# Kernel optimization log

Measured on AMD Instinct MI355X. Metric: run time of the kernel, lower is better.

The kernel has to match this reference:

```python
import jax, jax.numpy as jnp
import numpy as np

N = 50000        # nodes
E = 800000       # edges
R = 8            # relations
G = 64           # g_dim
H1 = 64          # h1_dim
H2 = 32          # h2_dim (per-head for transformer, output for sage)
HEADS = 4
EPS = 1e-5       # BatchNorm eps


def setup_inputs() -> dict:
    key = jax.random.key(0)
    ks = jax.random.split(key, 16)
    def rn(k, shape, scale=0.05):
        return jax.random.normal(k, shape, dtype=jnp.float32) * scale
    return {
        "node_features": jax.random.normal(ks[0], (N, G), dtype=jnp.float32),
        "node_type": jax.random.randint(ks[1], (N,), 0, 3),
        "edge_index": jax.random.randint(ks[2], (2, E), 0, N),
        "edge_type": jax.random.randint(ks[3], (E,), 0, R),
        # RGCNConv params (per-relation weight + root weight + bias)
        "rgcn_w": rn(ks[4], (R, G, H1)),
        "rgcn_root": rn(ks[5], (G, H1)),
        "rgcn_bias": jnp.zeros((H1,), jnp.float32),
        "bn1_g": jnp.ones((H1,), jnp.float32),
        "bn1_b": jnp.zeros((H1,), jnp.float32),
        # TransformerConv params (q/k/v projections + skip)
        "wq": rn(ks[6], (H1, HEADS * H2)), "bq": jnp.zeros((HEADS * H2,), jnp.float32),
        "wk": rn(ks[7], (H1, HEADS * H2)), "bk": jnp.zeros((HEADS * H2,), jnp.float32),
        "wv": rn(ks[8], (H1, HEADS * H2)), "bv": jnp.zeros((HEADS * H2,), jnp.float32),
        "wskip": rn(ks[9], (H1, HEADS * H2)), "bskip": jnp.zeros((HEADS * H2,), jnp.float32),
        "bn2_g": jnp.ones((HEADS * H2,), jnp.float32),
        "bn2_b": jnp.zeros((HEADS * H2,), jnp.float32),
        # SAGEConv params (lin_l on aggregated neighbors has bias; lin_r on root has none)
        "sage_wl": rn(ks[10], (HEADS * H2, H2)), "sage_bl": jnp.zeros((H2,), jnp.float32),
        "sage_wr": rn(ks[11], (HEADS * H2, H2)),
        "bn3_g": jnp.ones((H2,), jnp.float32),
        "bn3_b": jnp.zeros((H2,), jnp.float32),
    }


def _bn(x, g, b):
    # BatchNorm1d in training mode: biased batch statistics over nodes
    m = x.mean(0)
    v = x.var(0)
    return g * (x - m) * jax.lax.rsqrt(v + EPS) + b


def _match(res, d):
    # F.pad(res, (0, d - c)): pads with zeros if d > c, truncates if d < c
    c = res.shape[1]
    if d > c:
        return jnp.pad(res, ((0, 0), (0, d - c)))
    return res[:, :d]


def _forward(node_features, rgcn_w, rgcn_root, rgcn_bias, bn1_g, bn1_b,
             wq, bq, wk, bk, wv, bv, wskip, bskip, bn2_g, bn2_b,
             sage_wl, sage_bl, sage_wr, bn3_g, bn3_b,
             edge_index, edge_type):
    src, dst = edge_index[0], edge_index[1]
    x = node_features
    residual = x

    # ---- RGCNConv: per-relation transform, per-relation mean aggregation, sum over relations ----
    xr = jnp.einsum('nf,rfh->nrh', x, rgcn_w)            # [N,R,H1]
    msg = xr[src, edge_type]                              # [E,H1]
    seg = dst * R + edge_type                             # segment per (node, relation)
    sums = jax.ops.segment_sum(msg, seg, num_segments=N * R)
    cnt = jax.ops.segment_sum(jnp.ones((E,), msg.dtype), seg, num_segments=N * R)
    agg = (sums / jnp.maximum(cnt, 1.0)[:, None]).reshape(N, R, H1).sum(1)
    h = agg + x @ rgcn_root + rgcn_bias
    h = jax.nn.leaky_relu(_bn(h, bn1_g, bn1_b))
    x = h + _match(residual, h.shape[1])
    residual = x

    # ---- TransformerConv: edge softmax attention, concat heads, + skip projection ----
    q = (x @ wq + bq).reshape(N, HEADS, H2)
    k = (x @ wk + bk).reshape(N, HEADS, H2)
    v = (x @ wv + bv).reshape(N, HEADS, H2)
    logits = (q[dst] * k[src]).sum(-1) / jnp.sqrt(jnp.float32(H2))  # [E,HEADS]
    mx = jax.ops.segment_max(logits, dst, num_segments=N)
    ex = jnp.exp(logits - mx[dst])
    den = jax.ops.segment_sum(ex, dst, num_segments=N)
    alpha = ex / jnp.maximum(den[dst], 1e-16)
    out = jax.ops.segment_sum(alpha[:, :, None] * v[src], dst, num_segments=N)
    h = out.reshape(N, HEADS * H2) + x @ wskip + bskip
    h = jax.nn.leaky_relu(_bn(h, bn2_g, bn2_b))
    x = h + _match(residual, h.shape[1])
    residual = x

    # ---- SAGEConv: mean neighbor aggregation + root transform ----
    nsum = jax.ops.segment_sum(x[src], dst, num_segments=N)
    ncnt = jax.ops.segment_sum(jnp.ones((E,), x.dtype), dst, num_segments=N)
    nmean = nsum / jnp.maximum(ncnt, 1.0)[:, None]
    h = nmean @ sage_wl + sage_bl + x @ sage_wr
    h = jax.nn.leaky_relu(_bn(h, bn3_g, bn3_b))
    return h + _match(residual, h.shape[1])


def reference(node_features, node_type, edge_index, edge_type,
              rgcn_w, rgcn_root, rgcn_bias, bn1_g, bn1_b,
              wq, bq, wk, bk, wv, bv, wskip, bskip, bn2_g, bn2_b,
              sage_wl, sage_bl, sage_wr, bn3_g, bn3_b):
    # node_type is unused by the original forward
    return _forward(node_features, rgcn_w, rgcn_root, rgcn_bias, bn1_g, bn1_b,
                    wq, bq, wk, bk, wv, bv, wskip, bskip, bn2_g, bn2_b,
                    sage_wl, sage_bl, sage_wr, bn3_g, bn3_b,
                    edge_index, edge_type)
```

## Files before the change

kernel.cpp:

```cpp
#include <hip/hip_runtime.h>
#include <stdint.h>

#define NN 50000
#define NE 800000
#define NR (NN*8)
#define SCAN_BS 512
#define NB2 782
#define INV_N (1.0f/50000.0f)
#define BN_EPS 1e-5f

typedef unsigned short ushort_t;
typedef unsigned char uchar_t;
typedef short bf16x8 __attribute__((ext_vector_type(8)));
typedef float f32x4 __attribute__((ext_vector_type(4)));
typedef float f32x2 __attribute__((ext_vector_type(2)));

__device__ __forceinline__ ushort_t f2bf(float f){
    unsigned int u = __float_as_uint(f);
    u += 0x7FFFu + ((u >> 16) & 1u);
    return (ushort_t)(u >> 16);
}
__device__ __forceinline__ float bf2f(ushort_t h){ return __uint_as_float(((unsigned int)h) << 16); }
__device__ __forceinline__ float bflo(unsigned int u){ return __uint_as_float(u << 16); }
__device__ __forceinline__ float bfhi(unsigned int u){ return __uint_as_float(u & 0xFFFF0000u); }

__device__ __forceinline__ unsigned int f4_to_fp8(float a, float b, float c, float d){
    int v = __builtin_amdgcn_cvt_pk_fp8_f32(a, b, 0, false);
    v = __builtin_amdgcn_cvt_pk_fp8_f32(c, d, v, true);
    return (unsigned int)v;
}
__device__ __forceinline__ void fp8_to_f4(unsigned int u, float& a, float& b, float& c, float& d){
    f32x2 lo = __builtin_amdgcn_cvt_pk_f32_fp8(u, false);
    f32x2 hi = __builtin_amdgcn_cvt_pk_f32_fp8(u, true);
    a = lo.x; b = lo.y; c = hi.x; d = hi.y;
}

__global__ void k_deg(const int* __restrict__ ei, const int* __restrict__ et,
                      int* __restrict__ deg, uint2* __restrict__ sr){
    int e = blockIdx.x*256 + threadIdx.x;
    if (e < NE){
        int seg = ei[NE + e]*8 + et[e];
        int rank = atomicAdd(&deg[seg], 1);
        uint2 o; o.x = (unsigned)seg; o.y = (unsigned)rank;
        sr[e] = o;
    }
}

__global__ void k_scan1(const int* __restrict__ deg, int* __restrict__ tmp, int* __restrict__ bsum){
    __shared__ int s[SCAN_BS];
    int t = threadIdx.x;
    int i = blockIdx.x*SCAN_BS + t;
    s[t] = (i < NR) ? deg[i] : 0;
    __syncthreads();
    for (int off = 1; off < SCAN_BS; off <<= 1){
        int add = (t >= off) ? s[t-off] : 0;
        __syncthreads();
        s[t] += add;
        __syncthreads();
    }
    if (i < NR) tmp[i] = s[t];
    if (t == SCAN_BS-1) bsum[blockIdx.x] = s[t];
}

__global__ void k_scan2(int* __restrict__ bsum){
    __shared__ int s[NB2];
    int t = threadIdx.x;
    if (t < NB2) s[t] = bsum[t];
    __syncthreads();
    if (t == 0){
        int acc = 0;
        for (int i = 0; i < NB2; ++i){ acc += s[i]; s[i] = acc; }
    }
    __syncthreads();
    if (t < NB2) bsum[t] = s[t];
}

__global__ void k_scan3(const int* __restrict__ tmp, const int* __restrict__ bsum, int* __restrict__ rs){
    int i = blockIdx.x*256 + threadIdx.x;
    if (i < NR){
        int b = i >> 9;
        int off = (b > 0) ? bsum[b-1] : 0;
        rs[i+1] = tmp[i] + off;
        if (i == 0) rs[0] = 0;
    }
}

__global__ void k_fill(const int* __restrict__ ei, const uint2* __restrict__ sr,
                       const int* __restrict__ rs, int* __restrict__ csr){
    int e = blockIdx.x*256 + threadIdx.x;
    if (e < NE){
        uint2 s = sr[e];
        csr[rs[s.x] + (int)s.y] = ei[e];
    }
}

__global__ void k_prep(const float* __restrict__ nf,
                       const float* __restrict__ rgcn_w, const float* __restrict__ root,
                       const float* __restrict__ wq, const float* __restrict__ wk,
                       const float* __restrict__ wv, const float* __restrict__ wsk,
                       const float* __restrict__ bq, const float* __restrict__ bk,
                       const float* __restrict__ bv, const float* __restrict__ bsk,
                       const float* __restrict__ wl, const float* __restrict__ wr,
                       ushort_t* __restrict__ xb, uchar_t* __restrict__ xb8,
                       ushort_t* __restrict__ Wcat,
                       ushort_t* __restrict__ Wt2, float* __restrict__ bcat,
                       ushort_t* __restrict__ Wsage){
    int i = blockIdx.x*256 + threadIdx.x;
    const int NXB = NN*16;
    if (i < NXB){
        float4 v = ((const float4*)nf)[i];
        ushort4 h;
        h.x = f2bf(v.x); h.y = f2bf(v.y); h.z = f2bf(v.z); h.w = f2bf(v.w);
        ((ushort4*)xb)[i] = h;
        ((unsigned int*)xb8)[i] = f4_to_fp8(v.x, v.y, v.z, v.w);
        return;
    }
    int j = i - NXB;
    if (j < 64*576){
        int h = j / 576, k = j - h*576;
        float v = (k < 512) ? rgcn_w[(size_t)k*64 + h] : root[(size_t)(k-512)*64 + h];
        Wcat[j] = f2bf(v);
    } else if (j < 64*576 + 512*64){
        int jj = j - 64*576;
        int c = jj >> 6, k = jj & 63;
        int mt = c >> 7, cc = c & 127;
        const float* W = (mt==0)?wq:(mt==1)?wk:(mt==2)?wv:wsk;
        Wt2[jj] = f2bf(W[(size_t)k*128 + cc]);
    } else if (j < 64*576 + 512*64 + 512){
        int c = j - (64*576 + 512*64);
        int mt = c >> 7, cc = c & 127;
        const float* B = (mt==0)?bq:(mt==1)?bk:(mt==2)?bv:bsk;
        bcat[c] = B[cc];
    } else if (j < 64*576 + 512*64 + 512 + 32*256){
        int jj = j - (64*576 + 512*64 + 512);
        int c = jj >> 8, k = jj & 255;
        float v = (k < 128) ? wr[(size_t)k*32 + c] : wl[(size_t)(k-128)*32 + c];
        Wsage[jj] = f2bf(v);
    }
}

__global__ __launch_bounds__(256) void rgcn_fused(const ushort_t* __restrict__ xb,
                                                  const uchar_t* __restrict__ xb8,
                                                  const int* __restrict__ rs,
                                                  const int* __restrict__ csr,
                                                  const ushort_t* __restrict__ Wcat,
                                                  const float* __restrict__ bias,
                                                  float* __restrict__ h1pre){
    __shared__ ushort_t Ml[16*520];
    int w = threadIdx.x >> 6, lane = threadIdx.x & 63;
    int quad = lane >> 4, l4 = lane & 15;
    int row0 = blockIdx.x * 16;
    int n0 = row0 + w*4;
    int rsel = (lane < 9 ? lane : 8);
    int rb = rs[n0*8 + rsel];
    int eb0 = __shfl(rb, 0);
    int dg0 = __shfl(rb, 8) - eb0;
    int idx = (lane < dg0) ? csr[eb0 + lane] : 0;
    for (int j = 0; j < 4; ++j){
        int lrow = (w*4 + j)*520;
        int ebase = __shfl(rb, 0);
        int enext = __shfl(rb, 8);
        int rb_next = 0, idxn = 0;
        if (j < 3){
            rb_next = rs[(n0 + j + 1)*8 + rsel];
            idxn = csr[min(enext + lane, NE - 1)];
        }
        int e0a = __shfl(rb, quad),     e1a = __shfl(rb, quad + 1);
        int e0b = __shfl(rb, quad + 4), e1b = __shfl(rb, quad + 5);
        int oa = e0a - ebase, la = e1a - e0a;
        int ob = e0b - ebase, lb = e1b - e0b;
        int ml = max(la, lb);
        ml = max(ml, __shfl_xor(ml, 16));
        ml = max(ml, __shfl_xor(ml, 32));
        float aa0=0.f, aa1=0.f, aa2=0.f, aa3=0.f;
        float ab0=0.f, ab1=0.f, ab2=0.f, ab3=0.f;
        for (int i = 0; i < ml; i += 4){
            int sA[4], sB[4];
            bool vA[4], vB[4];
#pragma unroll
            for (int u = 0; u < 4; ++u){
                int jA = oa + i + u, jB = ob + i + u;
                vA[u] = (i + u) < la;
                vB[u] = (i + u) < lb;
                int tA = __shfl(idx, jA & 63);
                int tB = __shfl(idx, jB & 63);
                if (jA >= 64 && vA[u]) tA = csr[ebase + jA];
                if (jB >= 64 && vB[u]) tB = csr[ebase + jB];
                sA[u] = vA[u] ? tA : 0;
                sB[u] = vB[u] ? tB : 0;
            }
            unsigned int uA[4], uB[4];
#pragma unroll
            for (int u = 0; u < 4; ++u){
                uA[u] = *(const unsigned int*)(xb8 + (size_t)sA[u]*64 + l4*4);
                uB[u] = *(const unsigned int*)(xb8 + (size_t)sB[u]*64 + l4*4);
            }
#pragma unroll
            for (int u = 0; u < 4; ++u){
                float f0,f1,f2,f3;
                fp8_to_f4(uA[u],f0,f1,f2,f3);
                if (vA[u]){ aa0+=f0; aa1+=f1; aa2+=f2; aa3+=f3; }
                fp8_to_f4(uB[u],f0,f1,f2,f3);
                if (vB[u]){ ab0+=f0; ab1+=f1; ab2+=f2; ab3+=f3; }
            }
        }
        float inva = 1.f / fmaxf((float)la, 1.f);
        float invb = 1.f / fmaxf((float)lb, 1.f);
        ushort4 oA, oB;
        oA.x = f2bf(aa0*inva); oA.y = f2bf(aa1*inva); oA.z = f2bf(aa2*inva); oA.w = f2bf(aa3*inva);
        oB.x = f2bf(ab0*invb); oB.y = f2bf(ab1*invb); oB.z = f2bf(ab2*invb); oB.w = f2bf(ab3*invb);
        *(ushort4*)&Ml[lrow + quad*64 + l4*4] = oA;
        *(ushort4*)&Ml[lrow + (quad + 4)*64 + l4*4] = oB;
        if (j < 3){
            rb = rb_next;
            int ebn = __shfl(rb, 0);
            int dgn = __shfl(rb, 8) - ebn;
            idx = (lane < dgn) ? idxn : 0;
        }
    }
    __syncthreads();
    int m = l4;
    f32x4 acc = {};
#pragma unroll
    for (int kt = 0; kt < 18; ++kt){
        int kk = kt*32 + quad*8;
        bf16x8 a;
        if (kt < 16) a = *(const bf16x8*)&Ml[m*520 + kk];
        else         a = *(const bf16x8*)(xb + (size_t)(row0 + m)*64 + (kk - 512));
        bf16x8 b = *(const bf16x8*)(Wcat + (size_t)(w*16 + m)*576 + kk);
        acc = __builtin_amdgcn_mfma_f32_16x16x32_bf16(a, b, acc, 0, 0, 0);
    }
    int col = w*16 + m;
    float bz = bias[col];
#pragma unroll
    for (int i = 0; i < 4; ++i){
        int rr = row0 + quad*4 + i;
        h1pre[(size_t)rr*64 + col] = acc[i] + bz;
    }
}

__global__ void bn1_finalize(const float* __restrict__ sums, const float* __restrict__ sumsq,
                             const float* __restrict__ g1, const float* __restrict__ b1,
                             float* __restrict__ A1, float* __restrict__ C1){
    int c = threadIdx.x;
    if (c < 64){
        float m = sums[c] * INV_N;
        float v = sumsq[c] * INV_N - m*m;
        float rsv = rsqrtf(fmaxf(v, 0.f) + BN_EPS);
        float A = rsv * g1[c];
        A1[c] = A;
        C1[c] = b1[c] - m * A;
    }
}

#define QS 132
#define BS 68
__global__ __launch_bounds__(256) void gemm_qkvs(const float* __restrict__ h1pre,
                                                 const float* __restrict__ nf,
                                                 const float* __restrict__ A1, const float* __restrict__ C1,
                                                 const ushort_t* __restrict__ Wt2,
                                                 const float* __restrict__ bcat,
                                                 ushort_t* __restrict__ qb,
                                                 uchar_t* __restrict__ kb8,
                                                 ushort_t* __restrict__ vb,
                                                 ushort_t* __restrict__ sb){
    __shared__ ushort_t Bs[256*BS];
    __shared__ ushort_t pl[4][16*QS];
    int w = threadIdx.x >> 6, lane = threadIdx.x & 63;
    int m = lane & 15, quad = lane >> 4;
    int r0 = blockIdx.x*64 + w*16;
    int cg = blockIdx.y;
    int row = r0 + m;
    {
        int t = threadIdx.x;
        const ushort_t* wsrc = Wt2 + (size_t)cg*256*64;
#pragma unroll
        for (int u0 = 0; u0 < 8; ++u0){
            int u = u0*256 + t;
            int r = u >> 3, c8 = (u & 7)*8;
            *(uint4*)&Bs[r*BS + c8] = *(const uint4*)(wsrc + u*8);
        }
    }
    bf16x8 afrag[2];
#pragma unroll
    for (int kt = 0; kt < 2; ++kt){
        int db = kt*32 + quad*8;
        bf16x8 f = (bf16x8){0,0,0,0,0,0,0,0};
        if (row < NN){
            float4 h0 = *(const float4*)(h1pre + (size_t)row*64 + db);
            float4 h1 = *(const float4*)(h1pre + (size_t)row*64 + db + 4);
            float4 n0 = *(const float4*)(nf + (size_t)row*64 + db);
            float4 n1 = *(const float4*)(nf + (size_t)row*64 + db + 4);
            float4 a0 = *(const float4*)(A1 + db);
            float4 a1 = *(const float4*)(A1 + db + 4);
            float4 c0 = *(const float4*)(C1 + db);
            float4 c1 = *(const float4*)(C1 + db + 4);
            float hh[8] = {h0.x,h0.y,h0.z,h0.w,h1.x,h1.y,h1.z,h1.w};
            float nn[8] = {n0.x,n0.y,n0.z,n0.w,n1.x,n1.y,n1.z,n1.w};
            float AA[8] = {a0.x,a0.y,a0.z,a0.w,a1.x,a1.y,a1.z,a1.w};
            float CC[8] = {c0.x,c0.y,c0.z,c0.w,c1.x,c1.y,c1.z,c1.w};
#pragma unroll
            for (int e = 0; e < 8; ++e){
                float y = fmaf(hh[e], AA[e], CC[e]);
                y = (y >= 0.f) ? y : 0.01f*y;
                f[e] = (short)f2bf(y + nn[e]);
            }
        }
        afrag[kt] = f;
    }
    __syncthreads();
    f32x4 acc[16] = {};
#pragma unroll
    for (int kt = 0; kt < 2; ++kt){
        int kk = kt*32 + quad*8;
#pragma unroll
        for (int ct = 0; ct < 16; ++ct){
            bf16x8 b = *(const bf16x8*)&Bs[(size_t)(ct*16 + m)*BS + kk];
            acc[ct] = __builtin_amdgcn_mfma_f32_16x16x32_bf16(afrag[kt], b, acc[ct], 0, 0, 0);
        }
    }
#pragma unroll
    for (int ct = 0; ct < 8; ++ct){
        int g = cg*256 + ct*16 + m;
        float bz = bcat[g];
        int cc = g & 127;
#pragma unroll
        for (int i = 0; i < 4; ++i)
            pl[w][(quad*4 + i)*QS + cc] = f2bf(acc[ct][i] + bz);
    }
    if (cg == 0){
#pragma unroll
        for (int t = 0; t < 4; ++t){
            int u = t*64 + lane;
            int r = u >> 4, c = (u & 15)*8;
            int gr = r0 + r;
            if (gr < NN) *(uint4*)(qb + (size_t)gr*128 + c) = *(const uint4*)&pl[w][r*QS + c];
        }
    } else {
#pragma unroll
        for (int t = 0; t < 4; ++t){
            int u = t*64 + lane;
            int r = u >> 4, c = (u & 15)*8;
            int gr = r0 + r;
            if (gr < NN) *(uint4*)(vb + (size_t)gr*128 + c) = *(const uint4*)&pl[w][r*QS + c];
        }
    }
#pragma unroll
    for (int ct = 8; ct < 16; ++ct){
        int g = cg*256 + ct*16 + m;
        float bz = bcat[g];
        int cc = g & 127;
#pragma unroll
        for (int i = 0; i < 4; ++i)
            pl[w][(quad*4 + i)*QS + cc] = f2bf(acc[ct][i] + bz);
    }
    if (cg == 0){
#pragma unroll
        for (int t = 0; t < 4; ++t){
            int u = t*64 + lane;
            int r = u >> 4, c = (u & 15)*8;
            int gr = r0 + r;
            if (gr < NN){
                uint4 kk4 = *(const uint4*)&pl[w][r*QS + c];
                uint2 o;
                o.x = f4_to_fp8(bflo(kk4.x), bfhi(kk4.x), bflo(kk4.y), bfhi(kk4.y));
                o.y = f4_to_fp8(bflo(kk4.z), bfhi(kk4.z), bflo(kk4.w), bfhi(kk4.w));
                *(uint2*)(kb8 + (size_t)gr*128 + c) = o;
            }
        }
    } else {
#pragma unroll
        for (int t = 0; t < 4; ++t){
            int u = t*64 + lane;
            int r = u >> 4, c = (u & 15)*8;
            int gr = r0 + r;
            if (gr < NN) *(uint4*)(sb + (size_t)gr*128 + c) = *(const uint4*)&pl[w][r*QS + c];
        }
    }
}

__global__ __launch_bounds__(256) void sage_gemm(const ushort_t* __restrict__ x2b,
                                                 const ushort_t* __restrict__ nmeanb,
                                                 const ushort_t* __restrict__ Wsage,
                                                 const float* __restrict__ bl,
                                                 float* __restrict__ h3){
    int wv = threadIdx.x >> 6, lane = threadIdx.x & 63;
    int r0 = blockIdx.x*64 + wv*16;
    int m = lane & 15, quad = lane >> 4;
    int row = r0 + m;
    f32x4 acc[2] = {};
#pragma unroll
    for (int kt = 0; kt < 8; ++kt){
        int kk = kt*32 + quad*8;
        bf16x8 a;
        if (row < NN){
            const ushort_t* ap = (kt < 4) ? (x2b + (size_t)row*128 + kk)
                                          : (nmeanb + (size_t)row*128 + (kk - 128));
            a = *(const bf16x8*)ap;
        } else {
            a = (bf16x8){0,0,0,0,0,0,0,0};
        }
#pragma unroll
        for (int ct = 0; ct < 2; ++ct){
            bf16x8 b = *(const bf16x8*)(Wsage + (size_t)(ct*16 + m)*256 + kk);
            acc[ct] = __builtin_amdgcn_mfma_f32_16x16x32_bf16(a, b, acc[ct], 0, 0, 0);
        }
    }
#pragma unroll
    for (int ct = 0; ct < 2; ++ct){
        int col = ct*16 + m;
        float bz = bl[col];
#pragma unroll
        for (int i = 0; i < 4; ++i){
            int rr = r0 + quad*4 + i;
            if (rr < NN) h3[(size_t)rr*32 + col] = acc[ct][i] + bz;
        }
    }
}

template<int C>
__global__ __launch_bounds__(256) void bn_stats(const float* __restrict__ X, int ld,
                                                float* __restrict__ sums, float* __restrict__ sumsq){
    __shared__ float s1[256], s2[256];
    int t = threadIdx.x;
    int c = t & (C-1);
    const int rpb = 256 / C;
    int r = blockIdx.x * rpb + (t / C);
    int rstride = gridDim.x * rpb;
    float a = 0.f, b = 0.f;
    for (; r < NN; r += rstride){
        float v = X[(size_t)r*ld + c];
        a += v; b += v*v;
    }
    s1[t] = a; s2[t] = b;
    __syncthreads();
    for (int off = 128; off >= C; off >>= 1){
        if (t < off){ s1[t] += s1[t+off]; s2[t] += s2[t+off]; }
        __syncthreads();
    }
    if (t < C){ atomicAdd(&sums[t], s1[t]); atomicAdd(&sumsq[t], s2[t]); }
}

__device__ __forceinline__ float bn_leaky(float z, float m, float rsv, float g, float b){
    float y = (z - m) * rsv * g + b;
    return y >= 0.f ? y : 0.01f * y;
}

__global__ void bn_apply2(const float* __restrict__ h2, const float* __restrict__ h1pre,
                          const float* __restrict__ nf,
                          const float* __restrict__ g1, const float* __restrict__ b1,
                          const float* __restrict__ s1, const float* __restrict__ q1,
                          const float* __restrict__ g2, const float* __restrict__ b2,
                          const float* __restrict__ s2, const float* __restrict__ q2,
                          float* __restrict__ x2r, ushort_t* __restrict__ x2b,
                          uchar_t* __restrict__ x28){
    int i = blockIdx.x*256 + threadIdx.x;
    if (i >= NN*128) return;
    int n = i >> 7, c = i & 127;
    float m2 = s2[c] * INV_N;
    float v2 = q2[c] * INV_N - m2*m2;
    float rsv2 = rsqrtf(fmaxf(v2, 0.f) + BN_EPS);
    float val = bn_leaky(h2[i], m2, rsv2, g2[c], b2[c]);
    if (c < 64){
        float m1 = s1[c] * INV_N;
        float v1 = q1[c] * INV_N - m1*m1;
        float rsv1 = rsqrtf(fmaxf(v1, 0.f) + BN_EPS);
        val += bn_leaky(h1pre[(size_t)n*64 + c], m1, rsv1, g1[c], b1[c]) + nf[(size_t)n*64 + c];
    }
    if (c < 32) x2r[(size_t)n*32 + c] = val;
    x2b[i] = f2bf(val);
    int p = __builtin_amdgcn_cvt_pk_fp8_f32(val, val, 0, false);
    x28[i] = (uchar_t)(p & 0xFF);
}

__global__ void bn_apply3(const float* __restrict__ h3, const float* __restrict__ x2r,
                          const float* __restrict__ g, const float* __restrict__ b,
                          const float* __restrict__ sums, const float* __restrict__ sumsq,
                          float* __restrict__ out){
    int i = blockIdx.x*256 + threadIdx.x;
    if (i >= NN*32) return;
    int c = i & 31;
    float m = sums[c] * INV_N;
    float v = sumsq[c] * INV_N - m*m;
    float rsv = rsqrtf(fmaxf(v, 0.f) + BN_EPS);
    out[i] = bn_leaky(h3[i], m, rsv, g[c], b[c]) + x2r[i];
}

__global__ __launch_bounds__(256) void attn_kernel(const ushort_t* __restrict__ qb,
                                                   const uchar_t* __restrict__ kb8,
                                                   const ushort_t* __restrict__ vb,
                                                   const ushort_t* __restrict__ sb,
                                                   const int* __restrict__ rs,
                                                   const int* __restrict__ csr,
                                                   float* __restrict__ h2){
    int w = threadIdx.x >> 6, lane = threadIdx.x & 63;
    int n = blockIdx.x*4 + w;
    if (n >= NN) return;
    int half = lane >> 5, l5 = lane & 31;
    int e0 = rs[n*8], e1 = rs[n*8 + 8];
    int deg = e1 - e0;
    uint2 qu = *(const uint2*)(qb + (size_t)n*128 + l5*4);
    uint2 sbv = *(const uint2*)(sb + (size_t)n*128 + l5*4);
    float q0 = bflo(qu.x), q1 = bfhi(qu.x), q2 = bflo(qu.y), q3 = bfhi(qu.y);
    const float scale = 0.17677669529663687f;
    int idx = 0;
    if (lane < deg) idx = csr[e0 + lane];
    int dcap = min(deg, 64);
    int nt = (dcap + 7) >> 3;
    float den = 0.f, a0 = 0.f, a1 = 0.f, a2 = 0.f, a3 = 0.f;
    for (int t = 0; t < nt; ++t){
        int i2 = t*8 + half*4;
        int j0 = i2, j1 = i2+1, j2 = i2+2, j3 = i2+3;
        bool v0 = j0 < dcap, v1 = j1 < dcap, v2 = j2 < dcap, v3 = j3 < dcap;
        int s0 = __shfl(idx, j0 & 63); s0 = v0 ? s0 : 0;
        int s1 = __shfl(idx, j1 & 63); s1 = v1 ? s1 : 0;
        int s2 = __shfl(idx, j2 & 63); s2 = v2 ? s2 : 0;
        int s3 = __shfl(idx, j3 & 63); s3 = v3 ? s3 : 0;
        unsigned int ku0 = *(const unsigned int*)(kb8 + (size_t)s0*128 + l5*4);
        unsigned int ku1 = *(const unsigned int*)(kb8 + (size_t)s1*128 + l5*4);
        unsigned int ku2 = *(const unsigned int*)(kb8 + (size_t)s2*128 + l5*4);
        unsigned int ku3 = *(const unsigned int*)(kb8 + (size_t)s3*128 + l5*4);
        uint2 vv0 = *(const uint2*)(vb + (size_t)s0*128 + l5*4);
        uint2 vv1 = *(const uint2*)(vb + (size_t)s1*128 + l5*4);
        uint2 vv2 = *(const uint2*)(vb + (size_t)s2*128 + l5*4);
        uint2 vv3 = *(const uint2*)(vb + (size_t)s3*128 + l5*4);
        float ka, kb_, kc, kd;
        fp8_to_f4(ku0, ka, kb_, kc, kd);
        float p0 = q0*ka + q1*kb_ + q2*kc + q3*kd;
        fp8_to_f4(ku1, ka, kb_, kc, kd);
        float p1 = q0*ka + q1*kb_ + q2*kc + q3*kd;
        fp8_to_f4(ku2, ka, kb_, kc, kd);
        float p2 = q0*ka + q1*kb_ + q2*kc + q3*kd;
        fp8_to_f4(ku3, ka, kb_, kc, kd);
        float p3 = q0*ka + q1*kb_ + q2*kc + q3*kd;
        p0 += __shfl_xor(p0, 1); p1 += __shfl_xor(p1, 1); p2 += __shfl_xor(p2, 1); p3 += __shfl_xor(p3, 1);
        p0 += __shfl_xor(p0, 2); p1 += __shfl_xor(p1, 2); p2 += __shfl_xor(p2, 2); p3 += __shfl_xor(p3, 2);
        p0 += __shfl_xor(p0, 4); p1 += __shfl_xor(p1, 4); p2 += __shfl_xor(p2, 4); p3 += __shfl_xor(p3, 4);
        float w0 = v0 ? __expf(p0 * scale) : 0.f;
        float w1 = v1 ? __expf(p1 * scale) : 0.f;
        float w2 = v2 ? __expf(p2 * scale) : 0.f;
        float w3 = v3 ? __expf(p3 * scale) : 0.f;
        den += w0 + w1 + w2 + w3;
        a0 += w0*bflo(vv0.x) + w1*bflo(vv1.x) + w2*bflo(vv2.x) + w3*bflo(vv3.x);
        a1 += w0*bfhi(vv0.x) + w1*bfhi(vv1.x) + w2*bfhi(vv2.x) + w3*bfhi(vv3.x);
        a2 += w0*bflo(vv0.y) + w1*bflo(vv1.y) + w2*bflo(vv2.y) + w3*bflo(vv3.y);
        a3 += w0*bfhi(vv0.y) + w1*bfhi(vv1.y) + w2*bfhi(vv2.y) + w3*bfhi(vv3.y);
    }
    for (int e = 64 + half; e < deg; e += 2){
        int s = csr[e0 + e];
        unsigned int ku = *(const unsigned int*)(kb8 + (size_t)s*128 + l5*4);
        uint2 vv = *(const uint2*)(vb + (size_t)s*128 + l5*4);
        float ka, kb_, kc, kd;
        fp8_to_f4(ku, ka, kb_, kc, kd);
        float p = q0*ka + q1*kb_ + q2*kc + q3*kd;
        p += __shfl_xor(p, 1);
        p += __shfl_xor(p, 2);
        p += __shfl_xor(p, 4);
        float wg = __expf(p * scale);
        den += wg;
        a0 += wg*bflo(vv.x); a1 += wg*bfhi(vv.x);
        a2 += wg*bflo(vv.y); a3 += wg*bfhi(vv.y);
    }
    den += __shfl_xor(den, 32);
    a0 += __shfl_xor(a0, 32); a1 += __shfl_xor(a1, 32);
    a2 += __shfl_xor(a2, 32); a3 += __shfl_xor(a3, 32);
    if (half == 0){
        float inv = (den > 0.f) ? 1.f/den : 0.f;
        float4 o;
        o.x = bflo(sbv.x) + a0*inv;
        o.y = bfhi(sbv.x) + a1*inv;
        o.z = bflo(sbv.y) + a2*inv;
        o.w = bfhi(sbv.y) + a3*inv;
        *(float4*)(h2 + (size_t)n*128 + l5*4) = o;
    }
}

__global__ __launch_bounds__(256) void sage_agg(const uchar_t* __restrict__ x28,
                                                const int* __restrict__ rs,
                                                const int* __restrict__ csr,
                                                ushort_t* __restrict__ nmeanb){
    int w = threadIdx.x >> 6, lane = threadIdx.x & 63;
    int n = blockIdx.x*4 + w;
    if (n >= NN) return;
    int half = lane >> 5, l5 = lane & 31;
    int e0 = rs[n*8], e1 = rs[n*8 + 8];
    int deg = e1 - e0;
    int idx = 0;
    if (lane < deg) idx = csr[e0 + lane];
    int dcap = min(deg, 64);
    int nt = (dcap + 7) >> 3;
    float a0 = 0.f, a1 = 0.f, a2 = 0.f, a3 = 0.f;
    for (int t = 0; t < nt; ++t){
        int i2 = t*8 + half*4;
        int j0 = i2, j1 = i2+1, j2 = i2+2, j3 = i2+3;
        bool v0 = j0 < dcap, v1 = j1 < dcap, v2 = j2 < dcap, v3 = j3 < dcap;
        int s0 = __shfl(idx, j0 & 63); s0 = v0 ? s0 : 0;
        int s1 = __shfl(idx, j1 & 63); s1 = v1 ? s1 : 0;
        int s2 = __shfl(idx, j2 & 63); s2 = v2 ? s2 : 0;
        int s3 = __shfl(idx, j3 & 63); s3 = v3 ? s3 : 0;
        unsigned int u0 = *(const unsigned int*)(x28 + (size_t)s0*128 + l5*4);
        unsigned int u1 = *(const unsigned int*)(x28 + (size_t)s1*128 + l5*4);
        unsigned int u2 = *(const unsigned int*)(x28 + (size_t)s2*128 + l5*4);
        unsigned int u3 = *(const unsigned int*)(x28 + (size_t)s3*128 + l5*4);
        float fa, fb, fc, fd;
        if (v0){ fp8_to_f4(u0, fa, fb, fc, fd); a0 += fa; a1 += fb; a2 += fc; a3 += fd; }
        if (v1){ fp8_to_f4(u1, fa, fb, fc, fd); a0 += fa; a1 += fb; a2 += fc; a3 += fd; }
        if (v2){ fp8_to_f4(u2, fa, fb, fc, fd); a0 += fa; a1 += fb; a2 += fc; a3 += fd; }
        if (v3){ fp8_to_f4(u3, fa, fb, fc, fd); a0 += fa; a1 += fb; a2 += fc; a3 += fd; }
    }
    for (int e = 64 + half; e < deg; e += 2){
        int s = csr[e0 + e];
        unsigned int u = *(const unsigned int*)(x28 + (size_t)s*128 + l5*4);
        float fa, fb, fc, fd;
        fp8_to_f4(u, fa, fb, fc, fd);
        a0 += fa; a1 += fb; a2 += fc; a3 += fd;
    }
    a0 += __shfl_xor(a0, 32); a1 += __shfl_xor(a1, 32);
    a2 += __shfl_xor(a2, 32); a3 += __shfl_xor(a3, 32);
    if (half == 0){
        float inv = 1.f / fmaxf((float)deg, 1.f);
        ushort4 o;
        o.x = f2bf(a0*inv); o.y = f2bf(a1*inv); o.z = f2bf(a2*inv); o.w = f2bf(a3*inv);
        *(ushort4*)(nmeanb + (size_t)n*128 + l5*4) = o;
    }
}

extern "C" void kernel_launch(void* const* d_in, const int* in_sizes, int n_in,
                              void* d_out, int out_size, void* d_ws, size_t ws_size,
                              hipStream_t stream){
    const float* nf      = (const float*)d_in[0];
    const int*   ei      = (const int*)d_in[2];
    const int*   et      = (const int*)d_in[3];
    const float* rgcn_w  = (const float*)d_in[4];
    const float* root    = (const float*)d_in[5];
    const float* rbias   = (const float*)d_in[6];
    const float* bn1g    = (const float*)d_in[7];
    const float* bn1b    = (const float*)d_in[8];
    const float* wq      = (const float*)d_in[9];
    const float* bq      = (const float*)d_in[10];
    const float* wk      = (const float*)d_in[11];
    const float* bk      = (const float*)d_in[12];
    const float* wv      = (const float*)d_in[13];
    const float* bv      = (const float*)d_in[14];
    const float* wsk     = (const float*)d_in[15];
    const float* bsk     = (const float*)d_in[16];
    const float* bn2g    = (const float*)d_in[17];
    const float* bn2b    = (const float*)d_in[18];
    const float* wl      = (const float*)d_in[19];
    const float* bl      = (const float*)d_in[20];
    const float* wr      = (const float*)d_in[21];
    const float* bn3g    = (const float*)d_in[22];
    const float* bn3b    = (const float*)d_in[23];
    float* out = (float*)d_out;

    char* base = (char*)d_ws;
    size_t off = 0;
    auto take = [&](size_t bytes) -> char* {
        char* p = base + off;
        off += (bytes + 255) & ~(size_t)255;
        return p;
    };
    int*      deg    = (int*)take((size_t)NR*4);
    float*    bns    = (float*)take(1024*4);
    char*     zend   = base + off;
    int*      rs     = (int*)take((size_t)(NR+1)*4);
    int*      tmp    = (int*)take((size_t)NR*4);
    int*      bsum   = (int*)take(1024*4);
    uint2*    sr     = (uint2*)take((size_t)NE*8);
    int*      csr    = (int*)take((size_t)NE*4);
    ushort_t* Wcat   = (ushort_t*)take(64*576*2);
    ushort_t* Wt2    = (ushort_t*)take(512*64*2);
    float*    bcat   = (float*)take(512*4);
    ushort_t* Wsage  = (ushort_t*)take(32*256*2);
    ushort_t* xb     = (ushort_t*)take((size_t)NN*64*2);
    uchar_t*  xb8    = (uchar_t*)take((size_t)NN*64);
    float*    h1pre  = (float*)take((size_t)NN*64*4);
    float*    h2     = (float*)take((size_t)NN*128*4);
    float*    x2r    = (float*)take((size_t)NN*32*4);
    ushort_t* sb     = (ushort_t*)take((size_t)NN*128*2);
    char*     bigA   = take((size_t)NN*512*2);
    if (off > ws_size) return;

    ushort_t* qb     = (ushort_t*)(bigA + (size_t)NN*128);
    ushort_t* vb     = (ushort_t*)(bigA + (size_t)NN*384);
    uchar_t*  kb8    = (uchar_t*)(bigA + (size_t)NN*640);
    ushort_t* x2b    = (ushort_t*)bigA;
    uchar_t*  x28    = (uchar_t*)(bigA + (size_t)NN*256);
    ushort_t* nmeanb = (ushort_t*)(bigA + (size_t)NN*512);
    float*    h3     = (float*)(bigA + (size_t)NN*768);

    hipMemsetAsync(deg, 0, (size_t)(zend - (char*)deg), stream);

    const int PREP_N = NN*16 + 64*576 + 512*64 + 512 + 32*256;
    k_prep <<<(PREP_N+255)/256, 256, 0, stream>>>(nf, rgcn_w, root, wq, wk, wv, wsk,
                                                  bq, bk, bv, bsk, wl, wr,
                                                  xb, xb8, Wcat, Wt2, bcat, Wsage);
    k_deg  <<<(NE+255)/256, 256, 0, stream>>>(ei, et, deg, sr);
    k_scan1<<<NB2, SCAN_BS, 0, stream>>>(deg, tmp, bsum);
    k_scan2<<<1, 1024, 0, stream>>>(bsum);
    k_scan3<<<(NR+255)/256, 256, 0, stream>>>(tmp, bsum, rs);
    k_fill <<<(NE+255)/256, 256, 0, stream>>>(ei, sr, rs, csr);

    const int NB4 = (NN + 3) / 4;
    const int NBG = (NN + 63) / 64;

    rgcn_fused<<<NN/16, 256, 0, stream>>>(xb, xb8, rs, csr, Wcat, rbias, h1pre);
    bn_stats<64><<<256, 256, 0, stream>>>(h1pre, 64, bns + 0, bns + 64);
    bn1_finalize<<<1, 64, 0, stream>>>(bns + 0, bns + 64, bn1g, bn1b, bns + 448, bns + 512);

    gemm_qkvs<<<dim3(NBG, 2), 256, 0, stream>>>(h1pre, nf, bns + 448, bns + 512,
                                                Wt2, bcat, qb, kb8, vb, sb);
    attn_kernel<<<NB4, 256, 0, stream>>>(qb, kb8, vb, sb, rs, csr, h2);
    bn_stats<128><<<256, 256, 0, stream>>>(h2, 128, bns + 128, bns + 256);
    bn_apply2<<<(NN*128+255)/256, 256, 0, stream>>>(h2, h1pre, nf,
                                                    bn1g, bn1b, bns + 0, bns + 64,
                                                    bn2g, bn2b, bns + 128, bns + 256,
                                                    x2r, x2b, x28);

    sage_agg<<<NB4, 256, 0, stream>>>(x28, rs, csr, nmeanb);
    sage_gemm<<<NBG, 256, 0, stream>>>(x2b, nmeanb, Wsage, bl, h3);
    bn_stats<32><<<256, 256, 0, stream>>>(h3, 32, bns + 384, bns + 416);
    bn_apply3<<<(NN*32+255)/256, 256, 0, stream>>>(h3, x2r, bn3g, bn3b, bns + 384, bns + 416, out);
}
```

Before: 407.0 us.

## Aggregate RGCN edges per block with LDS atomics and fold BN1 finalize into GEMM

The CSR entries now carry the relation id in the high 16 bits, so the RGCN kernel can give each thread a quarter-row of an edge across the block's full edge range. Each thread accumulates into shared-memory float buffers with atomics instead of walking per-(node,relation) segments one warp at a time. This is meant to remove load imbalance and divergence from irregular per-relation degrees, at the cost of many LDS atomics. The separate bn1_finalize launch is dropped; each gemm_qkvs block computes the BN1 scale and shift into shared memory. Other consumers of the CSR mask off the relation bits.

```diff
diff --git a/kernel.cpp b/kernel.cpp
--- a/kernel.cpp
+++ b/kernel.cpp
@@ -90,7 +90,7 @@
     int e = blockIdx.x*256 + threadIdx.x;
     if (e < NE){
         uint2 s = sr[e];
-        csr[rs[s.x] + (int)s.y] = ei[e];
+        csr[rs[s.x] + (int)s.y] = ((int)(s.x & 7u) << 16) | ei[e];
     }
 }
 
@@ -146,77 +146,58 @@
                                                   const ushort_t* __restrict__ Wcat,
                                                   const float* __restrict__ bias,
                                                   float* __restrict__ h1pre){
-    __shared__ ushort_t Ml[16*520];
-    int w = threadIdx.x >> 6, lane = threadIdx.x & 63;
+    __shared__ float Macc[16*512];
+    __shared__ int   cnt[16*8];
+    __shared__ int   nb[17];
+    ushort_t* Ml = (ushort_t*)Macc;
+    int tid = threadIdx.x;
+    int w = tid >> 6, lane = tid & 63;
     int quad = lane >> 4, l4 = lane & 15;
     int row0 = blockIdx.x * 16;
-    int n0 = row0 + w*4;
-    int rsel = (lane < 9 ? lane : 8);
-    int rb = rs[n0*8 + rsel];
-    int eb0 = __shfl(rb, 0);
-    int dg0 = __shfl(rb, 8) - eb0;
-    int idx = (lane < dg0) ? csr[eb0 + lane] : 0;
-    for (int j = 0; j < 4; ++j){
-        int lrow = (w*4 + j)*520;
-        int ebase = __shfl(rb, 0);
-        int enext = __shfl(rb, 8);
-        int rb_next = 0, idxn = 0;
-        if (j < 3){
-            rb_next = rs[(n0 + j + 1)*8 + rsel];
-            idxn = csr[min(enext + lane, NE - 1)];
-        }
-        int e0a = __shfl(rb, quad),     e1a = __shfl(rb, quad + 1);
-        int e0b = __shfl(rb, quad + 4), e1b = __shfl(rb, quad + 5);
-        int oa = e0a - ebase, la = e1a - e0a;
-        int ob = e0b - ebase, lb = e1b - e0b;
-        int ml = max(la, lb);
-        ml = max(ml, __shfl_xor(ml, 16));
-        ml = max(ml, __shfl_xor(ml, 32));
-        float aa0=0.f, aa1=0.f, aa2=0.f, aa3=0.f;
-        float ab0=0.f, ab1=0.f, ab2=0.f, ab3=0.f;
-        for (int i = 0; i < ml; i += 4){
-            int sA[4], sB[4];
-            bool vA[4], vB[4];
-#pragma unroll
-            for (int u = 0; u < 4; ++u){
-                int jA = oa + i + u, jB = ob + i + u;
-                vA[u] = (i + u) < la;
-                vB[u] = (i + u) < lb;
-                int tA = __shfl(idx, jA & 63);
-                int tB = __shfl(idx, jB & 63);
-                if (jA >= 64 && vA[u]) tA = csr[ebase + jA];
-                if (jB >= 64 && vB[u]) tB = csr[ebase + jB];
-                sA[u] = vA[u] ? tA : 0;
-                sB[u] = vB[u] ? tB : 0;
-            }
-            unsigned int uA[4], uB[4];
-#pragma unroll
-            for (int u = 0; u < 4; ++u){
-                uA[u] = *(const unsigned int*)(xb8 + (size_t)sA[u]*64 + l4*4);
-                uB[u] = *(const unsigned int*)(xb8 + (size_t)sB[u]*64 + l4*4);
-            }
-#pragma unroll
-            for (int u = 0; u < 4; ++u){
-                float f0,f1,f2,f3;
-                fp8_to_f4(uA[u],f0,f1,f2,f3);
-                if (vA[u]){ aa0+=f0; aa1+=f1; aa2+=f2; aa3+=f3; }
-                fp8_to_f4(uB[u],f0,f1,f2,f3);
-                if (vB[u]){ ab0+=f0; ab1+=f1; ab2+=f2; ab3+=f3; }
-            }
-        }
-        float inva = 1.f / fmaxf((float)la, 1.f);
-        float invb = 1.f / fmaxf((float)lb, 1.f);
-        ushort4 oA, oB;
-        oA.x = f2bf(aa0*inva); oA.y = f2bf(aa1*inva); oA.z = f2bf(aa2*inva); oA.w = f2bf(aa3*inva);
-        oB.x = f2bf(ab0*invb); oB.y = f2bf(ab1*invb); oB.z = f2bf(ab2*invb); oB.w = f2bf(ab3*invb);
-        *(ushort4*)&Ml[lrow + quad*64 + l4*4] = oA;
-        *(ushort4*)&Ml[lrow + (quad + 4)*64 + l4*4] = oB;
-        if (j < 3){
-            rb = rb_next;
-            int ebn = __shfl(rb, 0);
-            int dgn = __shfl(rb, 8) - ebn;
-            idx = (lane < dgn) ? idxn : 0;
-        }
+    if (tid < 17) nb[tid] = rs[(row0 + tid)*8];
+    for (int i = tid; i < 16*512; i += 256) Macc[i] = 0.f;
+    if (tid < 128) cnt[tid] = 0;
+    __syncthreads();
+    int ebase = nb[0], eend = nb[16];
+    int ch0 = (tid & 3)*16;
+    for (int e = ebase + (tid >> 2); e < eend; e += 64){
+        int p = csr[e];
+        int src = p & 0xFFFF, rel = p >> 16;
+        int lo = 0;
+        if (e >= nb[lo + 8]) lo += 8;
+        if (e >= nb[lo + 4]) lo += 4;
+        if (e >= nb[lo + 2]) lo += 2;
+        if (e >= nb[lo + 1]) lo += 1;
+        uint4 u = *(const uint4*)(xb8 + (size_t)src*64 + ch0);
+        float* dst = &Macc[lo*512 + rel*64 + ch0];
+        float f0,f1,f2,f3;
+        fp8_to_f4(u.x, f0,f1,f2,f3);
+        atomicAdd(dst+0, f0); atomicAdd(dst+1, f1); atomicAdd(dst+2, f2); atomicAdd(dst+3, f3);
+        fp8_to_f4(u.y, f0,f1,f2,f3);
+        atomicAdd(dst+4, f0); atomicAdd(dst+5, f1); atomicAdd(dst+6, f2); atomicAdd(dst+7, f3);
+        fp8_to_f4(u.z, f0,f1,f2,f3);
+        atomicAdd(dst+8, f0); atomicAdd(dst+9, f1); atomicAdd(dst+10, f2); atomicAdd(dst+11, f3);
+        fp8_to_f4(u.w, f0,f1,f2,f3);
+        atomicAdd(dst+12, f0); atomicAdd(dst+13, f1); atomicAdd(dst+14, f2); atomicAdd(dst+15, f3);
+        if ((tid & 3) == 0) atomicAdd(&cnt[lo*8 + rel], 1);
+    }
+    __syncthreads();
+    unsigned int pk[16];
+#pragma unroll
+    for (int k = 0; k < 16; ++k){
+        int pi = tid + k*256;
+        int node = pi >> 8, chp = pi & 255, ch = chp*2;
+        float inv = 1.f / fmaxf((float)cnt[node*8 + (ch >> 6)], 1.f);
+        float v0 = Macc[node*512 + ch] * inv;
+        float v1 = Macc[node*512 + ch + 1] * inv;
+        pk[k] = (unsigned int)f2bf(v0) | ((unsigned int)f2bf(v1) << 16);
+    }
+    __syncthreads();
+#pragma unroll
+    for (int k = 0; k < 16; ++k){
+        int pi = tid + k*256;
+        int node = pi >> 8, ch = (pi & 255)*2;
+        *(unsigned int*)&Ml[node*520 + ch] = pk[k];
     }
     __syncthreads();
     int m = l4;
@@ -239,25 +220,12 @@
     }
 }
 
-__global__ void bn1_finalize(const float* __restrict__ sums, const float* __restrict__ sumsq,
-                             const float* __restrict__ g1, const float* __restrict__ b1,
-                             float* __restrict__ A1, float* __restrict__ C1){
-    int c = threadIdx.x;
-    if (c < 64){
-        float m = sums[c] * INV_N;
-        float v = sumsq[c] * INV_N - m*m;
-        float rsv = rsqrtf(fmaxf(v, 0.f) + BN_EPS);
-        float A = rsv * g1[c];
-        A1[c] = A;
-        C1[c] = b1[c] - m * A;
-    }
-}
-
 #define QS 132
 #define BS 68
 __global__ __launch_bounds__(256) void gemm_qkvs(const float* __restrict__ h1pre,
                                                  const float* __restrict__ nf,
-                                                 const float* __restrict__ A1, const float* __restrict__ C1,
+                                                 const float* __restrict__ s1, const float* __restrict__ q1,
+                                                 const float* __restrict__ g1, const float* __restrict__ b1,
                                                  const ushort_t* __restrict__ Wt2,
                                                  const float* __restrict__ bcat,
                                                  ushort_t* __restrict__ qb,
@@ -266,6 +234,7 @@
                                                  ushort_t* __restrict__ sb){
     __shared__ ushort_t Bs[256*BS];
     __shared__ ushort_t pl[4][16*QS];
+    __shared__ float A1s[64], C1s[64];
     int w = threadIdx.x >> 6, lane = threadIdx.x & 63;
     int m = lane & 15, quad = lane >> 4;
     int r0 = blockIdx.x*64 + w*16;
@@ -280,7 +249,16 @@
             int r = u >> 3, c8 = (u & 7)*8;
             *(uint4*)&Bs[r*BS + c8] = *(const uint4*)(wsrc + u*8);
         }
-    }
+        if (t < 64){
+            float mm = s1[t] * INV_N;
+            float vv = q1[t] * INV_N - mm*mm;
+            float rsv = rsqrtf(fmaxf(vv, 0.f) + BN_EPS);
+            float A = rsv * g1[t];
+            A1s[t] = A;
+            C1s[t] = b1[t] - mm * A;
+        }
+    }
+    __syncthreads();
     bf16x8 afrag[2];
 #pragma unroll
     for (int kt = 0; kt < 2; ++kt){
@@ -291,24 +269,18 @@
             float4 h1 = *(const float4*)(h1pre + (size_t)row*64 + db + 4);
             float4 n0 = *(const float4*)(nf + (size_t)row*64 + db);
             float4 n1 = *(const float4*)(nf + (size_t)row*64 + db + 4);
-            float4 a0 = *(const float4*)(A1 + db);
-            float4 a1 = *(const float4*)(A1 + db + 4);
-            float4 c0 = *(const float4*)(C1 + db);
-            float4 c1 = *(const float4*)(C1 + db + 4);
             float hh[8] = {h0.x,h0.y,h0.z,h0.w,h1.x,h1.y,h1.z,h1.w};
             float nn[8] = {n0.x,n0.y,n0.z,n0.w,n1.x,n1.y,n1.z,n1.w};
-            float AA[8] = {a0.x,a0.y,a0.z,a0.w,a1.x,a1.y,a1.z,a1.w};
-            float CC[8] = {c0.x,c0.y,c0.z,c0.w,c1.x,c1.y,c1.z,c1.w};
 #pragma unroll
             for (int e = 0; e < 8; ++e){
-                float y = fmaf(hh[e], AA[e], CC[e]);
+                int c = db + e;
+                float y = fmaf(hh[e], A1s[c], C1s[c]);
                 y = (y >= 0.f) ? y : 0.01f*y;
                 f[e] = (short)f2bf(y + nn[e]);
             }
         }
         afrag[kt] = f;
     }
-    __syncthreads();
     f32x4 acc[16] = {};
 #pragma unroll
     for (int kt = 0; kt < 2; ++kt){
@@ -512,10 +484,10 @@
         int i2 = t*8 + half*4;
         int j0 = i2, j1 = i2+1, j2 = i2+2, j3 = i2+3;
         bool v0 = j0 < dcap, v1 = j1 < dcap, v2 = j2 < dcap, v3 = j3 < dcap;
-        int s0 = __shfl(idx, j0 & 63); s0 = v0 ? s0 : 0;
-        int s1 = __shfl(idx, j1 & 63); s1 = v1 ? s1 : 0;
-        int s2 = __shfl(idx, j2 & 63); s2 = v2 ? s2 : 0;
-        int s3 = __shfl(idx, j3 & 63); s3 = v3 ? s3 : 0;
+        int s0 = __shfl(idx, j0 & 63) & 0xFFFF; s0 = v0 ? s0 : 0;
+        int s1 = __shfl(idx, j1 & 63) & 0xFFFF; s1 = v1 ? s1 : 0;
+        int s2 = __shfl(idx, j2 & 63) & 0xFFFF; s2 = v2 ? s2 : 0;
+        int s3 = __shfl(idx, j3 & 63) & 0xFFFF; s3 = v3 ? s3 : 0;
         unsigned int ku0 = *(const unsigned int*)(kb8 + (size_t)s0*128 + l5*4);
         unsigned int ku1 = *(const unsigned int*)(kb8 + (size_t)s1*128 + l5*4);
         unsigned int ku2 = *(const unsigned int*)(kb8 + (size_t)s2*128 + l5*4);
@@ -547,7 +519,7 @@
         a3 += w0*bfhi(vv0.y) + w1*bfhi(vv1.y) + w2*bfhi(vv2.y) + w3*bfhi(vv3.y);
     }
     for (int e = 64 + half; e < deg; e += 2){
-        int s = csr[e0 + e];
+        int s = csr[e0 + e] & 0xFFFF;
         unsigned int ku = *(const unsigned int*)(kb8 + (size_t)s*128 + l5*4);
         uint2 vv = *(const uint2*)(vb + (size_t)s*128 + l5*4);
         float ka, kb_, kc, kd;
@@ -594,10 +566,10 @@
         int i2 = t*8 + half*4;
         int j0 = i2, j1 = i2+1, j2 = i2+2, j3 = i2+3;
         bool v0 = j0 < dcap, v1 = j1 < dcap, v2 = j2 < dcap, v3 = j3 < dcap;
-        int s0 = __shfl(idx, j0 & 63); s0 = v0 ? s0 : 0;
-        int s1 = __shfl(idx, j1 & 63); s1 = v1 ? s1 : 0;
-        int s2 = __shfl(idx, j2 & 63); s2 = v2 ? s2 : 0;
-        int s3 = __shfl(idx, j3 & 63); s3 = v3 ? s3 : 0;
+        int s0 = __shfl(idx, j0 & 63) & 0xFFFF; s0 = v0 ? s0 : 0;
+        int s1 = __shfl(idx, j1 & 63) & 0xFFFF; s1 = v1 ? s1 : 0;
+        int s2 = __shfl(idx, j2 & 63) & 0xFFFF; s2 = v2 ? s2 : 0;
+        int s3 = __shfl(idx, j3 & 63) & 0xFFFF; s3 = v3 ? s3 : 0;
         unsigned int u0 = *(const unsigned int*)(x28 + (size_t)s0*128 + l5*4);
         unsigned int u1 = *(const unsigned int*)(x28 + (size_t)s1*128 + l5*4);
         unsigned int u2 = *(const unsigned int*)(x28 + (size_t)s2*128 + l5*4);
@@ -609,7 +581,7 @@
         if (v3){ fp8_to_f4(u3, fa, fb, fc, fd); a0 += fa; a1 += fb; a2 += fc; a3 += fd; }
     }
     for (int e = 64 + half; e < deg; e += 2){
-        int s = csr[e0 + e];
+        int s = csr[e0 + e] & 0xFFFF;
         unsigned int u = *(const unsigned int*)(x28 + (size_t)s*128 + l5*4);
         float fa, fb, fc, fd;
         fp8_to_f4(u, fa, fb, fc, fd);
@@ -706,9 +678,8 @@
 
     rgcn_fused<<<NN/16, 256, 0, stream>>>(xb, xb8, rs, csr, Wcat, rbias, h1pre);
     bn_stats<64><<<256, 256, 0, stream>>>(h1pre, 64, bns + 0, bns + 64);
-    bn1_finalize<<<1, 64, 0, stream>>>(bns + 0, bns + 64, bn1g, bn1b, bns + 448, bns + 512);
-
-    gemm_qkvs<<<dim3(NBG, 2), 256, 0, stream>>>(h1pre, nf, bns + 448, bns + 512,
+
+    gemm_qkvs<<<dim3(NBG, 2), 256, 0, stream>>>(h1pre, nf, bns + 0, bns + 64, bn1g, bn1b,
                                                 Wt2, bcat, qb, kb8, vb, sb);
     attn_kernel<<<NB4, 256, 0, stream>>>(qb, kb8, vb, sb, rs, csr, h2);
     bn_stats<128><<<256, 256, 0, stream>>>(h2, 128, bns + 128, bns + 256);
```

Result: slower. 649.6 us (+59.6%).
